# Kernel tuning notes

Hardware: AMD Instinct MI355X
Metric: run time of the kernel (lower is better)

## Reference

```python
import jax, jax.numpy as jnp
import numpy as np

B, L = 8, 512
EMB, NHEAD, HD = 512, 8, 64
FFN, NL = 2048, 6
VOCAB, NRE, RING_START, PAD, MAXLEN = 45, 20, 24, 0, 512
NOUT0 = VOCAB - NRE  # 25
NEG = -jnp.inf


def _ln(x, g, b, eps=1e-5):
    m = jnp.mean(x, -1, keepdims=True)
    v = jnp.mean((x - m) ** 2, -1, keepdims=True)
    return (x - m) * jax.lax.rsqrt(v + eps) * g + b


def setup_inputs():
    key = jax.random.key(0)
    ks = jax.random.split(key, 24)
    p = lambda k, shape: jax.random.normal(k, shape, jnp.float32) * 0.02
    return {
        "sequences": jax.random.randint(ks[0], (B, L), 1, VOCAB),  # avoid PAD=0
        "count_sequences": jax.random.randint(ks[1], (B, L), 0, MAXLEN),
        "graph_mask_sequences": jax.random.bernoulli(ks[2], 0.05, (B, L, VOCAB)),
        "valence_mask_sequences": jax.random.bernoulli(ks[3], 0.05, (B, L, VOCAB)),
        "linear_loc_squares": jax.random.randint(ks[4], (B, L, L), 0, MAXLEN + 1),
        "up_loc_squares": jax.random.randint(ks[5], (B, L, L), 0, MAXLEN + 1),
        "down_loc_squares": jax.random.randint(ks[6], (B, L, L), 0, MAXLEN + 1),
        "tok_emb": p(ks[7], (VOCAB, EMB)),
        "cnt_emb": p(ks[8], (MAXLEN, EMB)),
        "lin_loc_emb": p(ks[9], (MAXLEN + 1, NHEAD)),
        "up_loc_emb": p(ks[10], (MAXLEN + 1, NHEAD)),
        "down_loc_emb": p(ks[11], (MAXLEN + 1, NHEAD)),
        "in_proj_w": p(ks[12], (NL, 3 * EMB, EMB)),
        "in_proj_b": jnp.zeros((NL, 3 * EMB), jnp.float32),
        "out_w": p(ks[13], (NL, EMB, EMB)),
        "out_b": jnp.zeros((NL, EMB), jnp.float32),
        "ln1_g": jnp.ones((NL, EMB), jnp.float32),
        "ln1_b": jnp.zeros((NL, EMB), jnp.float32),
        "ln2_g": jnp.ones((NL, EMB), jnp.float32),
        "ln2_b": jnp.zeros((NL, EMB), jnp.float32),
        "ffn_w1": p(ks[14], (NL, FFN, EMB)),
        "ffn_b1": jnp.zeros((NL, FFN), jnp.float32),
        "ffn_w2": p(ks[15], (NL, EMB, FFN)),
        "ffn_b2": jnp.zeros((NL, EMB), jnp.float32),
        "fin_g": jnp.ones((EMB,), jnp.float32),
        "fin_b": jnp.zeros((EMB,), jnp.float32),
        "gen_w": p(ks[16], (NOUT0, EMB)),
        "gen_b": jnp.zeros((NOUT0,), jnp.float32),
        "ring_w0": p(ks[17], (EMB, EMB)),
        "ring_b0": jnp.zeros((EMB,), jnp.float32),
        "ring_w1": p(ks[18], (EMB, EMB)),
        "ring_b1": jnp.zeros((EMB,), jnp.float32),
    }


def _forward(tok_emb, cnt_emb, lin_loc_emb, up_loc_emb, down_loc_emb,
             in_proj_w, in_proj_b, out_w, out_b, ln1_g, ln1_b, ln2_g, ln2_b,
             ffn_w1, ffn_b1, ffn_w2, ffn_b2, fin_g, fin_b, gen_w, gen_b,
             ring_w0, ring_b0, ring_w1, ring_b1,
             sequences, count_sequences, graph_mask_sequences,
             valence_mask_sequences, linear_loc_squares, up_loc_squares,
             down_loc_squares):
    scale_e = jnp.sqrt(jnp.float32(EMB))
    x = tok_emb[sequences] * scale_e + cnt_emb[count_sequences] * scale_e  # (B,L,E)

    # per-head additive attention bias from three (B,L,L) index lookups
    bias = lin_loc_emb[linear_loc_squares] + up_loc_emb[up_loc_squares] + down_loc_emb[down_loc_squares]  # (B,L,L,H)
    bias = jnp.transpose(bias, (0, 3, 1, 2))  # (B,H,Lq,Lk)
    causal = jnp.tril(jnp.ones((L, L), bool))
    attn_bias = jnp.where(causal[None, None], bias, NEG)
    pad = sequences == PAD  # key padding
    attn_bias = jnp.where(pad[:, None, None, :], NEG, attn_bias)

    inv_sqrt_hd = 1.0 / jnp.sqrt(jnp.float32(HD))
    for i in range(NL):  # post-norm TransformerEncoderLayer, gelu
        qkv = jnp.einsum('ble,fe->blf', x, in_proj_w[i]) + in_proj_b[i]
        q, k, v = jnp.split(qkv, 3, axis=-1)
        q = q.reshape(B, L, NHEAD, HD)
        k = k.reshape(B, L, NHEAD, HD)
        v = v.reshape(B, L, NHEAD, HD)
        scores = jnp.einsum('bqhd,bkhd->bhqk', q, k) * inv_sqrt_hd + attn_bias
        a = jax.nn.softmax(scores, axis=-1)
        ctx = jnp.einsum('bhqk,bkhd->bqhd', a, v).reshape(B, L, EMB)
        attn_out = jnp.einsum('ble,fe->blf', ctx, out_w[i]) + out_b[i]
        x = _ln(x + attn_out, ln1_g[i], ln1_b[i])
        h = jax.nn.gelu(jnp.einsum('ble,fe->blf', x, ffn_w1[i]) + ffn_b1[i], approximate=False)
        ff = jnp.einsum('blf,ef->ble', h, ffn_w2[i]) + ffn_b2[i]
        x = _ln(x + ff, ln2_g[i], ln2_b[i])
    x = _ln(x, fin_g, fin_b)

    logits0 = jnp.einsum('ble,oe->blo', x, gen_w) + gen_b  # (B,L,NOUT0)

    # EdgeLogitLayer: scatter ring-start projections into NRE slots
    out0 = jnp.einsum('ble,he->blh', x, ring_w0) + ring_b0
    out1_ = jnp.einsum('ble,he->blh', x, ring_w1) + ring_b1
    ring_start = sequences == RING_START
    idx = jnp.where(ring_start, jnp.cumsum(ring_start.astype(jnp.int32), axis=1), 0)  # (B,L)
    bidx = jnp.arange(B)[:, None]
    slots = jnp.zeros((B, NRE + 1, EMB), x.dtype).at[bidx, idx].set(out1_, mode='drop')
    ring_tab = slots[:, 1:]  # drop slot 0 (non-ring-start writes)
    logits1 = jnp.einsum('ble,bre->blr', out0, ring_tab) * (EMB ** -0.5)

    logits = jnp.concatenate([logits0, logits1], axis=2)  # (B,L,VOCAB)
    logits = jnp.where(graph_mask_sequences, NEG, logits)
    logits = jnp.where(valence_mask_sequences, NEG, logits)
    return logits


def reference(sequences, count_sequences, graph_mask_sequences, valence_mask_sequences,
              linear_loc_squares, up_loc_squares, down_loc_squares,
              tok_emb, cnt_emb, lin_loc_emb, up_loc_emb, down_loc_emb,
              in_proj_w, in_proj_b, out_w, out_b, ln1_g, ln1_b, ln2_g, ln2_b,
              ffn_w1, ffn_b1, ffn_w2, ffn_b2, fin_g, fin_b, gen_w, gen_b,
              ring_w0, ring_b0, ring_w1, ring_b1):
    return _forward(tok_emb, cnt_emb, lin_loc_emb, up_loc_emb, down_loc_emb,
                    in_proj_w, in_proj_b, out_w, out_b, ln1_g, ln1_b, ln2_g, ln2_b,
                    ffn_w1, ffn_b1, ffn_w2, ffn_b2, fin_g, fin_b, gen_w, gen_b,
                    ring_w0, ring_b0, ring_w1, ring_b1,
                    sequences, count_sequences, graph_mask_sequences,
                    valence_mask_sequences, linear_loc_squares, up_loc_squares,
                    down_loc_squares)
```

## Files before the change

### kernel.cpp

```cpp
#include <hip/hip_runtime.h>
#include <cmath>

#define BB 8
#define LL 512
#define EMB 512
#define NHEAD 8
#define HD 64
#define FFN 2048
#define NL 6
#define VOCAB 45
#define NRE 20
#define RING_START 24
#define NOUT0 25
#define BL 4096

#define BIG_NEG -1.0e30f

typedef __bf16 bf16x8 __attribute__((ext_vector_type(8)));
typedef __bf16 bf16x4 __attribute__((ext_vector_type(4)));
typedef float f32x4 __attribute__((ext_vector_type(4)));

__device__ __forceinline__ void ld_g2l(const __bf16* g, __bf16* l) {
  __builtin_amdgcn_global_load_lds(
      (const __attribute__((address_space(1))) unsigned int*)g,
      (__attribute__((address_space(3))) unsigned int*)l, 16, 0, 0);
}

__global__ __launch_bounds__(256) void megacast_kernel(
    const float* __restrict__ s0, const float* __restrict__ s1,
    const float* __restrict__ s2, const float* __restrict__ s3,
    const float* __restrict__ s4, const float* __restrict__ s5,
    const float* __restrict__ s6, const float* __restrict__ s7,
    const float* __restrict__ s8, __bf16* __restrict__ dw,
    __bf16* __restrict__ dt) {
  const int gid = blockIdx.x * 256 + threadIdx.x;
  const int szs[9] = {589824, 196608, 786432, 786432, 32768,
                      32768,  513,    513,    513};
  const float* srcs[9] = {s0, s1, s2, s3, s4, s5, s6, s7, s8};
  int seg = 0, base = 0;
  while (seg < 9 && gid >= base + szs[seg]) { base += szs[seg]; seg++; }
  if (seg >= 9) return;
  const int local = gid - base;
  const float* src = srcs[seg];
  const float4 a = ((const float4*)src)[local * 2];
  const float4 b = ((const float4*)src)[local * 2 + 1];
  bf16x8 v;
  v[0] = (__bf16)a.x; v[1] = (__bf16)a.y; v[2] = (__bf16)a.z; v[3] = (__bf16)a.w;
  v[4] = (__bf16)b.x; v[5] = (__bf16)b.y; v[6] = (__bf16)b.z; v[7] = (__bf16)b.w;
  __bf16* dst = (seg < 6) ? (dw + (size_t)base * 8 + (size_t)local * 8)
                          : (dt + (size_t)(seg - 6) * 4104 + (size_t)local * 8);
  *(bf16x8*)dst = v;
}

__global__ __launch_bounds__(128) void embed_kernel(
    const int* __restrict__ seq, const int* __restrict__ cnt,
    const float* __restrict__ tok_emb, const float* __restrict__ cnt_emb,
    float* __restrict__ x, __bf16* __restrict__ xb) {
  const int row = blockIdx.x;
  const int t = seq[row];
  const int c = cnt[row];
  const float scale = 22.627416997969522f;
  const int j = threadIdx.x * 4;
  float4 tv = *(const float4*)(tok_emb + (size_t)t * EMB + j);
  float4 cv = *(const float4*)(cnt_emb + (size_t)c * EMB + j);
  float4 o;
  o.x = (tv.x + cv.x) * scale;
  o.y = (tv.y + cv.y) * scale;
  o.z = (tv.z + cv.z) * scale;
  o.w = (tv.w + cv.w) * scale;
  *(float4*)(x + (size_t)row * EMB + j) = o;
  bf16x4 h;
  h[0] = (__bf16)o.x; h[1] = (__bf16)o.y; h[2] = (__bf16)o.z; h[3] = (__bf16)o.w;
  *(bf16x4*)(xb + (size_t)row * EMB + j) = h;
}

__global__ __launch_bounds__(256) void bias_kernel(
    const int* __restrict__ lin_sq, const int* __restrict__ up_sq,
    const int* __restrict__ down_sq,
    const __bf16* __restrict__ tl16, const __bf16* __restrict__ tu16,
    const __bf16* __restrict__ td16,
    const int* __restrict__ seq, __bf16* __restrict__ bias) {
  __shared__ __bf16 Tl[513 * 8], Tu[513 * 8], Td[513 * 8];
  __shared__ int seqs[LL];
  const int tid = threadIdx.x;
  const int b = blockIdx.x >> 6;
  const int q0 = (blockIdx.x & 63) * 8;
  for (int i = tid; i < 513; i += 256) {
    *(bf16x8*)&Tl[i * 8] = *(const bf16x8*)&tl16[i * 8];
    *(bf16x8*)&Tu[i * 8] = *(const bf16x8*)&tu16[i * 8];
    *(bf16x8*)&Td[i * 8] = *(const bf16x8*)&td16[i * 8];
  }
  for (int i = tid; i < LL; i += 256) seqs[i] = seq[b * LL + i];
  __syncthreads();
  for (int q = q0; q < q0 + 8; q++) {
    const size_t rbase = ((size_t)(b * LL + q)) * LL;
    for (int k = tid; k <= q; k += 256) {
      const int li = lin_sq[rbase + k], ui = up_sq[rbase + k],
                di = down_sq[rbase + k];
      const bool valid = (seqs[k] != 0);
      bf16x8 a = *(const bf16x8*)&Tl[li * 8];
      bf16x8 u = *(const bf16x8*)&Tu[ui * 8];
      bf16x8 d = *(const bf16x8*)&Td[di * 8];
#pragma unroll
      for (int h = 0; h < NHEAD; h++) {
        float v = valid ? ((float)a[h] + (float)u[h] + (float)d[h])
                        : -INFINITY;
        bias[(((size_t)(b * NHEAD + h) * LL) + q) * LL + k] = (__bf16)v;
      }
    }
  }
}

template <int BM, int BN, int ACT, int OUTBF, int RES, int B2>
__global__ __launch_bounds__(256) void gemm_mfma_kernel(
    const __bf16* __restrict__ A, const __bf16* __restrict__ W,
    const float* __restrict__ bias, const float* __restrict__ bias2,
    float* __restrict__ C, __bf16* __restrict__ Cb,
    const float* __restrict__ Res, int N, int K, int lda) {
  constexpr int MI = BM / 32;
  constexpr int NI = BN / 32;
  __shared__ __bf16 As[BM * 64];
  __shared__ __bf16 Ws[BN * 64];
  const int tid = threadIdx.x;
  const int lane = tid & 63, wave = tid >> 6;
  const int wm = wave >> 1, wn = wave & 1;
  const int q = lane >> 4, l15 = lane & 15;
  const int m0 = blockIdx.y * BM, n0 = blockIdx.x * BN;

  const int sr = tid >> 3;
  const int sc = (tid & 7) ^ (sr & 7);
  const __bf16* Ag = A + (size_t)(m0 + sr) * lda + sc * 8;
  const __bf16* Wg = W + (size_t)(n0 + sr) * lda + sc * 8;
  __bf16* Al = &As[tid * 8];
  __bf16* Wl = &Ws[tid * 8];

  f32x4 acc[MI][NI] = {};

  for (int k0 = 0; k0 < K; k0 += 64) {
    ld_g2l(Ag + k0, Al);
    ld_g2l(Ag + k0 + (size_t)32 * lda, Al + 2048);
    if (BM == 128) {
      ld_g2l(Ag + k0 + (size_t)64 * lda, Al + 4096);
      ld_g2l(Ag + k0 + (size_t)96 * lda, Al + 6144);
    }
    ld_g2l(Wg + k0, Wl);
    ld_g2l(Wg + k0 + (size_t)32 * lda, Wl + 2048);
    if (BN == 128) {
      ld_g2l(Wg + k0 + (size_t)64 * lda, Wl + 4096);
      ld_g2l(Wg + k0 + (size_t)96 * lda, Wl + 6144);
    }
    __syncthreads();
#pragma unroll
    for (int kh = 0; kh < 2; kh++) {
      bf16x8 af[MI], bfr[NI];
      const int ch = ((kh * 4 + q) ^ (l15 & 7)) * 8;
#pragma unroll
      for (int mi = 0; mi < MI; mi++)
        af[mi] =
            *(const bf16x8*)&As[(wm * (BM / 2) + mi * 16 + l15) * 64 + ch];
#pragma unroll
      for (int ni = 0; ni < NI; ni++)
        bfr[ni] =
            *(const bf16x8*)&Ws[(wn * (BN / 2) + ni * 16 + l15) * 64 + ch];
#pragma unroll
      for (int mi = 0; mi < MI; mi++)
#pragma unroll
        for (int ni = 0; ni < NI; ni++)
          acc[mi][ni] = __builtin_amdgcn_mfma_f32_16x16x32_bf16(
              af[mi], bfr[ni], acc[mi][ni], 0, 0, 0);
    }
    __syncthreads();
  }

#pragma unroll
  for (int ni = 0; ni < NI; ni++) {
    const int n = n0 + wn * (BN / 2) + ni * 16 + l15;
    const float bv = (B2 && n >= EMB) ? bias2[n - EMB] : bias[n];
#pragma unroll
    for (int mi = 0; mi < MI; mi++) {
#pragma unroll
      for (int r = 0; r < 4; r++) {
        const int m = m0 + wm * (BM / 2) + mi * 16 + q * 4 + r;
        float v = acc[mi][ni][r] + bv;
        if (RES) v += Res[(size_t)m * N + n];
        if (ACT == 1) v = 0.5f * v * (1.0f + erff(v * 0.70710678118654752f));
        if (OUTBF)
          Cb[(size_t)m * N + n] = (__bf16)v;
        else
          C[(size_t)m * N + n] = v;
      }
    }
  }
}

__global__ __launch_bounds__(256) void attn_tile2_kernel(
    const __bf16* __restrict__ qkv, const __bf16* __restrict__ bias,
    __bf16* __restrict__ Po, float2* __restrict__ Pml) {
  __shared__ __bf16 Ks[64][72];
  __shared__ __bf16 Vt[64][72];
  __shared__ __bf16 Ps[64][72];
  const int tid = threadIdx.x;
  const int lane = tid & 63, w = tid >> 6;
  const int q = lane >> 4, l15 = lane & 15;
  const int bh = blockIdx.y;
  const int b = bh >> 3, h = bh & 7;
  const int pidx = blockIdx.x;
  int qt = 0, acc0 = 0;
  while (acc0 + (qt / 2 + 1) <= pidx) { acc0 += qt / 2 + 1; qt++; }
  const int j = pidx - acc0;
  const int q0 = qt * 64;
  const int slot = (bh * 8 + qt) * 4 + j;
  const float inv_sqrt_hd = 0.125f;

  const int srow = tid >> 2, c0 = (tid & 3) * 16;
  {
    const __bf16* qsrc =
        qkv + (size_t)(b * LL + q0 + srow) * 1536 + h * HD + c0;
    *(bf16x8*)&Ps[srow][c0] = *(const bf16x8*)qsrc;
    *(bf16x8*)&Ps[srow][c0 + 8] = *(const bf16x8*)(qsrc + 8);
  }
  __syncthreads();
  const bf16x8 aq0 = *(const bf16x8*)&Ps[w * 16 + l15][q * 8];
  const bf16x8 aq1 = *(const bf16x8*)&Ps[w * 16 + l15][32 + q * 8];

  f32x4 o4[4] = {};
  float m[4], l[4];
#pragma unroll
  for (int r = 0; r < 4; r++) { m[r] = -INFINITY; l[r] = 0.f; }

  const int ktEnd = (2 * j + 1 <= qt) ? (2 * j + 1) : qt;
  for (int kt = 2 * j; kt <= ktEnd; kt++) {
    const int k0 = kt * 64;
    __syncthreads();
    {
      const __bf16* src = qkv + (size_t)(b * LL + k0 + srow) * 1536 + h * HD;
      bf16x8 kv0 = *(const bf16x8*)(src + 512 + c0);
      bf16x8 kv1 = *(const bf16x8*)(src + 512 + c0 + 8);
      bf16x8 vv0 = *(const bf16x8*)(src + 1024 + c0);
      bf16x8 vv1 = *(const bf16x8*)(src + 1024 + c0 + 8);
      *(bf16x8*)&Ks[srow][c0] = kv0;
      *(bf16x8*)&Ks[srow][c0 + 8] = kv1;
#pragma unroll
      for (int jj = 0; jj < 8; jj++) {
        Vt[c0 + jj][srow] = vv0[jj];
        Vt[c0 + 8 + jj][srow] = vv1[jj];
      }
    }
    __syncthreads();

    f32x4 s4[4] = {};
#pragma unroll
    for (int ni = 0; ni < 4; ni++) {
      bf16x8 bk0 = *(const bf16x8*)&Ks[ni * 16 + l15][q * 8];
      bf16x8 bk1 = *(const bf16x8*)&Ks[ni * 16 + l15][32 + q * 8];
      s4[ni] =
          __builtin_amdgcn_mfma_f32_16x16x32_bf16(aq0, bk0, s4[ni], 0, 0, 0);
      s4[ni] =
          __builtin_amdgcn_mfma_f32_16x16x32_bf16(aq1, bk1, s4[ni], 0, 0, 0);
    }

    const bool diag = (kt == qt);
    const size_t bbase = ((size_t)bh * LL + (q0 + w * 16 + q * 4)) * LL + k0;
#pragma unroll
    for (int r = 0; r < 4; r++) {
      const int qrow = w * 16 + q * 4 + r;
      float sv[4];
#pragma unroll
      for (int ni = 0; ni < 4; ni++) {
        sv[ni] = s4[ni][r] * inv_sqrt_hd +
                 (float)bias[bbase + (size_t)r * LL + ni * 16 + l15];
        if (diag && (ni * 16 + l15 > qrow)) sv[ni] = -INFINITY;
      }
      float tm = fmaxf(fmaxf(sv[0], sv[1]), fmaxf(sv[2], sv[3]));
#pragma unroll
      for (int off = 1; off < 16; off <<= 1)
        tm = fmaxf(tm, __shfl_xor(tm, off, 16));
      const float mnew = fmaxf(m[r], tm);
      const float alpha = expf(m[r] - mnew);
      float rs = 0.f;
#pragma unroll
      for (int ni = 0; ni < 4; ni++) {
        const float p = expf(sv[ni] - mnew);
        Ps[qrow][ni * 16 + l15] = (__bf16)p;
        rs += p;
      }
#pragma unroll
      for (int off = 1; off < 16; off <<= 1) rs += __shfl_xor(rs, off, 16);
      l[r] = l[r] * alpha + rs;
      m[r] = mnew;
#pragma unroll
      for (int ni = 0; ni < 4; ni++) o4[ni][r] *= alpha;
    }
    __syncthreads();

    {
      bf16x8 ap0 = *(const bf16x8*)&Ps[w * 16 + l15][q * 8];
      bf16x8 ap1 = *(const bf16x8*)&Ps[w * 16 + l15][32 + q * 8];
#pragma unroll
      for (int ni = 0; ni < 4; ni++) {
        bf16x8 bv0 = *(const bf16x8*)&Vt[ni * 16 + l15][q * 8];
        bf16x8 bv1 = *(const bf16x8*)&Vt[ni * 16 + l15][32 + q * 8];
        o4[ni] =
            __builtin_amdgcn_mfma_f32_16x16x32_bf16(ap0, bv0, o4[ni], 0, 0, 0);
        o4[ni] =
            __builtin_amdgcn_mfma_f32_16x16x32_bf16(ap1, bv1, o4[ni], 0, 0, 0);
      }
    }
  }

#pragma unroll
  for (int r = 0; r < 4; r++) {
    const int qrow = w * 16 + q * 4 + r;
    if (l15 == 0)
      Pml[(size_t)slot * 64 + qrow] = make_float2(m[r], l[r]);
    __bf16* dst = Po + (size_t)slot * 4096 + qrow * 64 + l15;
#pragma unroll
    for (int ni = 0; ni < 4; ni++) dst[ni * 16] = (__bf16)o4[ni][r];
  }
}

__global__ __launch_bounds__(256) void attn_combine_kernel(
    const __bf16* __restrict__ Po, const float2* __restrict__ Pml,
    __bf16* __restrict__ ctx) {
  const int tid = threadIdx.x;
  const int bh = blockIdx.x >> 3;
  const int qt = blockIdx.x & 7;
  const int b = bh >> 3, h = bh & 7;
  const int nsl = qt / 2 + 1;
  const int slot0 = blockIdx.x * 4;
  __shared__ float wls[4][64];
  __shared__ float invl[64];
  if (tid < 64) {
    float mg = -3.0e38f;
    for (int s = 0; s < nsl; s++)
      mg = fmaxf(mg, Pml[(size_t)(slot0 + s) * 64 + tid].x);
    float lsum = 0.f;
    for (int s = 0; s < nsl; s++) {
      const float2 ml = Pml[(size_t)(slot0 + s) * 64 + tid];
      const float wk = expf(ml.x - mg);
      wls[s][tid] = wk;
      lsum += ml.y * wk;
    }
    invl[tid] = 1.0f / lsum;
  }
  __syncthreads();
  const int row = tid >> 2, d0 = (tid & 3) * 16;
  float acc[16] = {};
  for (int s = 0; s < nsl; s++) {
    const __bf16* src = Po + (size_t)(slot0 + s) * 4096 + row * 64 + d0;
    const float wk = wls[s][row];
    bf16x8 v0 = *(const bf16x8*)src;
    bf16x8 v1 = *(const bf16x8*)(src + 8);
#pragma unroll
    for (int jj = 0; jj < 8; jj++) {
      acc[jj] += (float)v0[jj] * wk;
      acc[8 + jj] += (float)v1[jj] * wk;
    }
  }
  const float il = invl[row];
  bf16x8 o0, o1;
#pragma unroll
  for (int jj = 0; jj < 8; jj++) {
    o0[jj] = (__bf16)(acc[jj] * il);
    o1[jj] = (__bf16)(acc[8 + jj] * il);
  }
  __bf16* dst = ctx + (size_t)(b * LL + qt * 64 + row) * EMB + h * HD + d0;
  *(bf16x8*)dst = o0;
  *(bf16x8*)(dst + 8) = o1;
}

template <int NSUM>
__global__ __launch_bounds__(256) void add_ln_kernel(
    const float* __restrict__ xin, const float* __restrict__ g,
    const float* __restrict__ bta, float* __restrict__ out,
    __bf16* __restrict__ outb) {
  const int row = blockIdx.x;
  const int tid = threadIdx.x;
  float v0 = 0.f, v1 = 0.f;
#pragma unroll
  for (int sId = 0; sId < NSUM; sId++) {
    const float* xr = xin + (size_t)sId * BL * EMB + (size_t)row * EMB;
    v0 += xr[tid * 2];
    v1 += xr[tid * 2 + 1];
  }
  float s = v0 + v1, ss = v0 * v0 + v1 * v1;
#pragma unroll
  for (int off = 1; off < 64; off <<= 1) {
    s += __shfl_xor(s, off, 64);
    ss += __shfl_xor(ss, off, 64);
  }
  __shared__ float sbuf[8];
  const int wave = tid >> 6, lane = tid & 63;
  if (lane == 0) { sbuf[wave] = s; sbuf[4 + wave] = ss; }
  __syncthreads();
  s = sbuf[0] + sbuf[1] + sbuf[2] + sbuf[3];
  ss = sbuf[4] + sbuf[5] + sbuf[6] + sbuf[7];
  const float mean = s * (1.0f / EMB);
  const float var = ss * (1.0f / EMB) - mean * mean;
  const float rstd = rsqrtf(var + 1e-5f);
  const float o0 = (v0 - mean) * rstd * g[tid * 2] + bta[tid * 2];
  const float o1 = (v1 - mean) * rstd * g[tid * 2 + 1] + bta[tid * 2 + 1];
  float* orow = out + (size_t)row * EMB;
  orow[tid * 2] = o0;
  orow[tid * 2 + 1] = o1;
  if (outb) {
    __bf16* brow = outb + (size_t)row * EMB;
    brow[tid * 2] = (__bf16)o0;
    brow[tid * 2 + 1] = (__bf16)o1;
  }
}

__global__ __launch_bounds__(256) void ring_scatter_kernel(
    const int* __restrict__ seq, const float* __restrict__ o01,
    float* __restrict__ ring_tab) {
  const int b = blockIdx.x;
  const int tid = threadIdx.x;
  float* rt = ring_tab + (size_t)b * NRE * EMB;
  for (int i = tid; i < NRE * EMB; i += 256) rt[i] = 0.f;
  __shared__ int pos[NRE];
  __shared__ int cntr;
  if (tid == 0) {
    int c = 0;
    for (int l = 0; l < LL; l++) {
      if (seq[b * LL + l] == RING_START) {
        c++;
        if (c <= NRE) pos[c - 1] = l;
      }
    }
    cntr = (c < NRE) ? c : NRE;
  }
  __syncthreads();
  const int n = cntr;
  for (int r = 0; r < n; r++) {
    const float* src = o01 + (size_t)(b * LL + pos[r]) * 1024 + 512;
    for (int i = tid; i < EMB; i += 256) rt[r * EMB + i] = src[i];
  }
}

__global__ __launch_bounds__(256) void head_kernel(
    const float* __restrict__ xf, const float* __restrict__ o01,
    const float* __restrict__ ring_tab, const float* __restrict__ gen_w,
    const float* __restrict__ gen_b, const int* __restrict__ gmask,
    const int* __restrict__ vmask, float* __restrict__ out) {
  const int row = blockIdx.x;
  const int b = row >> 9;
  const int tid = threadIdx.x;
  __shared__ float xr[EMB], o0s[EMB];
  {
    float2 a = ((const float2*)(xf + (size_t)row * EMB))[tid];
    ((float2*)xr)[tid] = a;
    float2 c = ((const float2*)(o01 + (size_t)row * 1024))[tid];
    ((float2*)o0s)[tid] = c;
  }
  __syncthreads();
  const int wave = tid >> 6, lane = tid & 63;
  for (int o = wave; o < VOCAB; o += 4) {
    const float* wrow;
    const float* src;
    float bv, scale;
    if (o < NOUT0) {
      wrow = gen_w + (size_t)o * EMB;
      bv = gen_b[o];
      src = xr;
      scale = 1.0f;
    } else {
      wrow = ring_tab + ((size_t)b * NRE + (o - NOUT0)) * EMB;
      bv = 0.0f;
      src = o0s;
      scale = 0.044194173824159216f;
    }
    float sum = 0.f;
#pragma unroll
    for (int j = 0; j < 8; j++) {
      const int d = lane + 64 * j;
      sum += src[d] * wrow[d];
    }
#pragma unroll
    for (int off = 1; off < 64; off <<= 1) sum += __shfl_xor(sum, off, 64);
    if (lane == 0) {
      float v = sum * scale + bv;
      const size_t oidx = (size_t)row * VOCAB + o;
      if (gmask[oidx] != 0 || vmask[oidx] != 0) v = BIG_NEG;
      out[oidx] = v;
    }
  }
}

extern "C" void kernel_launch(void* const* d_in, const int* in_sizes, int n_in,
                              void* d_out, int out_size, void* d_ws,
                              size_t ws_size, hipStream_t stream) {
  const int* seq = (const int*)d_in[0];
  const int* cnt = (const int*)d_in[1];
  const int* gmask = (const int*)d_in[2];
  const int* vmask = (const int*)d_in[3];
  const int* lin_sq = (const int*)d_in[4];
  const int* up_sq = (const int*)d_in[5];
  const int* down_sq = (const int*)d_in[6];
  const float* tok_emb = (const float*)d_in[7];
  const float* cnt_emb = (const float*)d_in[8];
  const float* lin_e = (const float*)d_in[9];
  const float* up_e = (const float*)d_in[10];
  const float* down_e = (const float*)d_in[11];
  const float* in_proj_w = (const float*)d_in[12];
  const float* in_proj_b = (const float*)d_in[13];
  const float* out_w = (const float*)d_in[14];
  const float* out_b = (const float*)d_in[15];
  const float* ln1_g = (const float*)d_in[16];
  const float* ln1_b = (const float*)d_in[17];
  const float* ln2_g = (const float*)d_in[18];
  const float* ln2_b = (const float*)d_in[19];
  const float* ffn_w1 = (const float*)d_in[20];
  const float* ffn_b1 = (const float*)d_in[21];
  const float* ffn_w2 = (const float*)d_in[22];
  const float* ffn_b2 = (const float*)d_in[23];
  const float* fin_g = (const float*)d_in[24];
  const float* fin_b = (const float*)d_in[25];
  const float* gen_w = (const float*)d_in[26];
  const float* gen_b = (const float*)d_in[27];
  const float* ring_w0 = (const float*)d_in[28];
  const float* ring_b0 = (const float*)d_in[29];
  const float* ring_w1 = (const float*)d_in[30];
  const float* ring_b1 = (const float*)d_in[31];

  char* p = (char*)d_ws;
  auto alloc_f = [&](size_t n) { float* r = (float*)p; p += n * 4; return r; };
  auto alloc_h = [&](size_t n) { __bf16* r = (__bf16*)p; p += n * 2; return r; };

  float* x = alloc_f((size_t)BL * EMB);
  float* pbuf = alloc_f((size_t)BL * EMB);
  float* xfb = alloc_f((size_t)BL * EMB);
  float* o01b = alloc_f((size_t)BL * 1024);
  float* ringb = alloc_f((size_t)BB * NRE * EMB);
  float2* attn_pml = (float2*)alloc_f((size_t)2048 * 64 * 2);
  __bf16* attn_po = alloc_h((size_t)2048 * 4096);
  __bf16* biasb = alloc_h((size_t)BB * NHEAD * LL * LL);
  __bf16* xb = alloc_h((size_t)BL * EMB);
  __bf16* qkvb16 = alloc_h((size_t)BL * 3 * EMB);
  __bf16* ctxb = alloc_h((size_t)BL * EMB);
  __bf16* hb = alloc_h((size_t)BL * FFN);
  __bf16* xfb16 = alloc_h((size_t)BL * EMB);
  __bf16* wqkv = alloc_h((size_t)NL * 3 * EMB * EMB);
  __bf16* wout = alloc_h((size_t)NL * EMB * EMB);
  __bf16* wf1 = alloc_h((size_t)NL * FFN * EMB);
  __bf16* wf2 = alloc_h((size_t)NL * EMB * FFN);
  __bf16* wr01 = alloc_h((size_t)2 * EMB * EMB);
  __bf16* tl16 = hb;
  __bf16* tu16 = hb + 4104;
  __bf16* td16 = hb + 8208;

  megacast_kernel<<<9478, 256, 0, stream>>>(
      in_proj_w, out_w, ffn_w1, ffn_w2, ring_w0, ring_w1, lin_e, up_e, down_e,
      wqkv, tl16);

  embed_kernel<<<BL, 128, 0, stream>>>(seq, cnt, tok_emb, cnt_emb, x, xb);
  bias_kernel<<<BB * 64, 256, 0, stream>>>(lin_sq, up_sq, down_sq, tl16, tu16,
                                           td16, seq, biasb);

  for (int i = 0; i < NL; i++) {
    gemm_mfma_kernel<64, 128, 0, 1, 0, 0><<<dim3(12, 64), 256, 0, stream>>>(
        xb, wqkv + (size_t)i * 3 * EMB * EMB, in_proj_b + (size_t)i * 3 * EMB,
        nullptr, nullptr, qkvb16, nullptr, 3 * EMB, EMB, EMB);
    attn_tile2_kernel<<<dim3(20, 64), 256, 0, stream>>>(qkvb16, biasb, attn_po,
                                                        attn_pml);
    attn_combine_kernel<<<512, 256, 0, stream>>>(attn_po, attn_pml, ctxb);
    gemm_mfma_kernel<64, 64, 0, 0, 1, 0><<<dim3(8, 64), 256, 0, stream>>>(
        ctxb, wout + (size_t)i * EMB * EMB, out_b + (size_t)i * EMB, nullptr,
        pbuf, nullptr, x, EMB, EMB, EMB);
    add_ln_kernel<1><<<BL, 256, 0, stream>>>(
        pbuf, ln1_g + (size_t)i * EMB, ln1_b + (size_t)i * EMB, x, xb);
    gemm_mfma_kernel<64, 128, 1, 1, 0, 0><<<dim3(16, 64), 256, 0, stream>>>(
        xb, wf1 + (size_t)i * FFN * EMB, ffn_b1 + (size_t)i * FFN, nullptr,
        nullptr, hb, nullptr, FFN, EMB, EMB);
    gemm_mfma_kernel<64, 64, 0, 0, 1, 0><<<dim3(8, 64), 256, 0, stream>>>(
        hb, wf2 + (size_t)i * EMB * FFN, ffn_b2 + (size_t)i * EMB, nullptr,
        pbuf, nullptr, x, EMB, FFN, FFN);
    add_ln_kernel<1><<<BL, 256, 0, stream>>>(
        pbuf, ln2_g + (size_t)i * EMB, ln2_b + (size_t)i * EMB, x, xb);
  }

  add_ln_kernel<1><<<BL, 256, 0, stream>>>(x, fin_g, fin_b, xfb, xfb16);
  gemm_mfma_kernel<64, 128, 0, 0, 0, 1><<<dim3(8, 64), 256, 0, stream>>>(
      xfb16, wr01, ring_b0, ring_b1, o01b, nullptr, nullptr, 1024, EMB, EMB);
  ring_scatter_kernel<<<BB, 256, 0, stream>>>(seq, o01b, ringb);
  head_kernel<<<BL, 256, 0, stream>>>(xfb, o01b, ringb, gen_w, gen_b, gmask,
                                      vmask, (float*)d_out);
}
```

Measured before the change: 920.9 us.

## Write single-split attention tiles directly, parallelize ring scatter, enlarge FFN1 tile

Query tiles 0 and 1 have only one key split, so the attention kernel now normalizes them and writes straight to the context buffer. The combine kernel launches only for query tiles 2-7. The ring scatter replaces a serial single-thread scan with a ballot and prefix-count using 512 threads. The first FFN GEMM moves to a 128x128 tile, halving the block count, which may lower occupancy or load balance.

```diff
diff --git a/kernel.cpp b/kernel.cpp
--- a/kernel.cpp
+++ b/kernel.cpp
@@ -195,7 +195,8 @@
 
 __global__ __launch_bounds__(256) void attn_tile2_kernel(
     const __bf16* __restrict__ qkv, const __bf16* __restrict__ bias,
-    __bf16* __restrict__ Po, float2* __restrict__ Pml) {
+    __bf16* __restrict__ Po, float2* __restrict__ Pml,
+    __bf16* __restrict__ ctx) {
   __shared__ __bf16 Ks[64][72];
   __shared__ __bf16 Vt[64][72];
   __shared__ __bf16 Ps[64][72];
@@ -210,6 +211,7 @@
   const int j = pidx - acc0;
   const int q0 = qt * 64;
   const int slot = (bh * 8 + qt) * 4 + j;
+  const bool direct = (qt <= 1);
   const float inv_sqrt_hd = 0.125f;
 
   const int srow = tid >> 2, c0 = (tid & 3) * 16;
@@ -308,14 +310,25 @@
     }
   }
 
-#pragma unroll
-  for (int r = 0; r < 4; r++) {
-    const int qrow = w * 16 + q * 4 + r;
-    if (l15 == 0)
-      Pml[(size_t)slot * 64 + qrow] = make_float2(m[r], l[r]);
-    __bf16* dst = Po + (size_t)slot * 4096 + qrow * 64 + l15;
-#pragma unroll
-    for (int ni = 0; ni < 4; ni++) dst[ni * 16] = (__bf16)o4[ni][r];
+  if (direct) {
+#pragma unroll
+    for (int r = 0; r < 4; r++) {
+      const int qrow = w * 16 + q * 4 + r;
+      const float inv = 1.0f / l[r];
+      __bf16* dst = ctx + (size_t)(b * LL + q0 + qrow) * EMB + h * HD + l15;
+#pragma unroll
+      for (int ni = 0; ni < 4; ni++) dst[ni * 16] = (__bf16)(o4[ni][r] * inv);
+    }
+  } else {
+#pragma unroll
+    for (int r = 0; r < 4; r++) {
+      const int qrow = w * 16 + q * 4 + r;
+      if (l15 == 0)
+        Pml[(size_t)slot * 64 + qrow] = make_float2(m[r], l[r]);
+      __bf16* dst = Po + (size_t)slot * 4096 + qrow * 64 + l15;
+#pragma unroll
+      for (int ni = 0; ni < 4; ni++) dst[ni * 16] = (__bf16)o4[ni][r];
+    }
   }
 }
 
@@ -323,11 +336,11 @@
     const __bf16* __restrict__ Po, const float2* __restrict__ Pml,
     __bf16* __restrict__ ctx) {
   const int tid = threadIdx.x;
-  const int bh = blockIdx.x >> 3;
-  const int qt = blockIdx.x & 7;
+  const int bh = blockIdx.x / 6;
+  const int qt = (blockIdx.x % 6) + 2;
   const int b = bh >> 3, h = bh & 7;
   const int nsl = qt / 2 + 1;
-  const int slot0 = blockIdx.x * 4;
+  const int slot0 = (bh * 8 + qt) * 4;
   __shared__ float wls[4][64];
   __shared__ float invl[64];
   if (tid < 64) {
@@ -410,30 +423,37 @@
   }
 }
 
-__global__ __launch_bounds__(256) void ring_scatter_kernel(
+__global__ __launch_bounds__(512) void ring_scatter_kernel(
     const int* __restrict__ seq, const float* __restrict__ o01,
     float* __restrict__ ring_tab) {
   const int b = blockIdx.x;
   const int tid = threadIdx.x;
   float* rt = ring_tab + (size_t)b * NRE * EMB;
-  for (int i = tid; i < NRE * EMB; i += 256) rt[i] = 0.f;
   __shared__ int pos[NRE];
-  __shared__ int cntr;
+  __shared__ int wcnt[8];
+  __shared__ int total;
+  const bool flag = (seq[b * LL + tid] == RING_START);
+  const unsigned long long msk = __ballot(flag);
+  const int wave = tid >> 6, lane = tid & 63;
+  if (lane == 0) wcnt[wave] = __popcll(msk);
+  for (int i = tid; i < NRE * EMB; i += 512) rt[i] = 0.f;
+  __syncthreads();
+  if (flag) {
+    int base = 0;
+    for (int w2 = 0; w2 < wave; w2++) base += wcnt[w2];
+    const int ord = base + __popcll(msk & ((1ull << lane) - 1ull));
+    if (ord < NRE) pos[ord] = tid;
+  }
   if (tid == 0) {
-    int c = 0;
-    for (int l = 0; l < LL; l++) {
-      if (seq[b * LL + l] == RING_START) {
-        c++;
-        if (c <= NRE) pos[c - 1] = l;
-      }
-    }
-    cntr = (c < NRE) ? c : NRE;
+    int t = 0;
+    for (int w2 = 0; w2 < 8; w2++) t += wcnt[w2];
+    total = (t < NRE) ? t : NRE;
   }
   __syncthreads();
-  const int n = cntr;
+  const int n = total;
   for (int r = 0; r < n; r++) {
     const float* src = o01 + (size_t)(b * LL + pos[r]) * 1024 + 512;
-    for (int i = tid; i < EMB; i += 256) rt[r * EMB + i] = src[i];
+    rt[r * EMB + tid] = src[tid];
   }
 }
 
@@ -561,14 +581,14 @@
         xb, wqkv + (size_t)i * 3 * EMB * EMB, in_proj_b + (size_t)i * 3 * EMB,
         nullptr, nullptr, qkvb16, nullptr, 3 * EMB, EMB, EMB);
     attn_tile2_kernel<<<dim3(20, 64), 256, 0, stream>>>(qkvb16, biasb, attn_po,
-                                                        attn_pml);
-    attn_combine_kernel<<<512, 256, 0, stream>>>(attn_po, attn_pml, ctxb);
+                                                        attn_pml, ctxb);
+    attn_combine_kernel<<<384, 256, 0, stream>>>(attn_po, attn_pml, ctxb);
     gemm_mfma_kernel<64, 64, 0, 0, 1, 0><<<dim3(8, 64), 256, 0, stream>>>(
         ctxb, wout + (size_t)i * EMB * EMB, out_b + (size_t)i * EMB, nullptr,
         pbuf, nullptr, x, EMB, EMB, EMB);
     add_ln_kernel<1><<<BL, 256, 0, stream>>>(
         pbuf, ln1_g + (size_t)i * EMB, ln1_b + (size_t)i * EMB, x, xb);
-    gemm_mfma_kernel<64, 128, 1, 1, 0, 0><<<dim3(16, 64), 256, 0, stream>>>(
+    gemm_mfma_kernel<128, 128, 1, 1, 0, 0><<<dim3(16, 32), 256, 0, stream>>>(
         xb, wf1 + (size_t)i * FFN * EMB, ffn_b1 + (size_t)i * FFN, nullptr,
         nullptr, hb, nullptr, FFN, EMB, EMB);
     gemm_mfma_kernel<64, 64, 0, 0, 1, 0><<<dim3(8, 64), 256, 0, stream>>>(
@@ -581,7 +601,7 @@
   add_ln_kernel<1><<<BL, 256, 0, stream>>>(x, fin_g, fin_b, xfb, xfb16);
   gemm_mfma_kernel<64, 128, 0, 0, 0, 1><<<dim3(8, 64), 256, 0, stream>>>(
       xfb16, wr01, ring_b0, ring_b1, o01b, nullptr, nullptr, 1024, EMB, EMB);
-  ring_scatter_kernel<<<BB, 256, 0, stream>>>(seq, o01b, ringb);
+  ring_scatter_kernel<<<BB, 512, 0, stream>>>(seq, o01b, ringb);
   head_kernel<<<BL, 256, 0, stream>>>(xfb, o01b, ringb, gen_w, gen_b, gmask,
                                       vmask, (float*)d_out);
 }
```

Result: no change. 911.8 us (-1.0%).
